# Performance work log

Hardware: AMD Instinct MI355X
Metric: run time of the kernel (lower is better)

Reference implementation:

```python
import jax, jax.numpy as jnp
import numpy as np

N = 8192
IN_FEATS = 512
OUT_FEATS = 64
NEG_SLOPE = 0.01  # torch nn.LeakyReLU default


def setup_inputs() -> dict:
    key = jax.random.key(0)
    k1, k2, k3, k4, k5, k6 = jax.random.split(key, 6)
    inputs = jax.random.normal(k1, (N, IN_FEATS), dtype=jnp.float32)
    adj_matrix = (jax.random.uniform(k2, (N, N)) < 0.01).astype(jnp.float32)
    eye_matrix = jnp.eye(N, dtype=jnp.float32)
    # nn.Linear params (torch default init: U(-1/sqrt(in), 1/sqrt(in)))
    bound = 1.0 / np.sqrt(IN_FEATS)
    W = jax.random.uniform(k3, (OUT_FEATS, IN_FEATS), minval=-bound, maxval=bound, dtype=jnp.float32)
    b = jax.random.uniform(k4, (OUT_FEATS,), minval=-bound, maxval=bound, dtype=jnp.float32)
    # a_1, a_2 init: torch.rand -> U(0,1)
    a1 = jax.random.uniform(k5, (1, OUT_FEATS), dtype=jnp.float32)
    a2 = jax.random.uniform(k6, (1, OUT_FEATS), dtype=jnp.float32)
    return {"inputs": inputs, "adj_matrix": adj_matrix, "eye_matrix": eye_matrix,
            "W": W, "b": b, "a1": a1, "a2": a2}


def reference(inputs, adj_matrix, eye_matrix, W, b, a1, a2):
    z = inputs @ W.T + b                              # (N, out_feats)
    zi = jnp.sum(a1 * z, axis=1, keepdims=True)       # (N, 1)
    zj = jnp.sum(a2 * z, axis=1, keepdims=True)       # (N, 1)
    attention_A = adj_matrix * zi                     # row-broadcast, (N, N)
    attention_B = adj_matrix * (eye_matrix * zj)      # (N, N)
    attn = jax.nn.leaky_relu(attention_A + attention_B, negative_slope=NEG_SLOPE)
    attn = jax.nn.softmax(attn, axis=1)               # (N, N)
    h = z - attn @ z                                  # (N, out_feats)
    return jax.nn.relu(h)
```

## Files before the change

kernel.cpp:

```cpp
#include <hip/hip_runtime.h>
#include <math.h>

#define N 8192
#define INF 512
#define OUTF 64
#define NEG_SLOPE 0.01f

typedef float f32x4 __attribute__((ext_vector_type(4)));

__global__ __launch_bounds__(256) void k1_linear(
    const float* __restrict__ inputs, const float* __restrict__ W,
    const float* __restrict__ b, const float* __restrict__ a1,
    const float* __restrict__ a2,
    float* __restrict__ z, float* __restrict__ zi, float* __restrict__ zj,
    float* __restrict__ ztot)
{
    const int tid = threadIdx.x;
    const int f   = tid & 63;
    const int w   = tid >> 6;
    const int row0 = blockIdx.x * 8;

    __shared__ float part[4][8][64];
    __shared__ float ztot_l[64];
    if (tid < 64) ztot_l[tid] = 0.0f;

    float acc[8];
    #pragma unroll
    for (int r = 0; r < 8; ++r) acc[r] = 0.0f;

    const f32x4* wrow = (const f32x4*)(W + (size_t)f * INF + w * 128);
    const f32x4* irow = (const f32x4*)(inputs + (size_t)row0 * INF + w * 128);

    #pragma unroll 4
    for (int k4 = 0; k4 < 32; ++k4) {
        const f32x4 wv = wrow[k4];
        #pragma unroll
        for (int r = 0; r < 8; ++r) {
            const f32x4 iv = irow[(size_t)r * (INF / 4) + k4];
            acc[r] += wv.x * iv.x + wv.y * iv.y + wv.z * iv.z + wv.w * iv.w;
        }
    }
    #pragma unroll
    for (int r = 0; r < 8; ++r) part[w][r][f] = acc[r];
    __syncthreads();

    const float bias = b[f];
    const float a1f = a1[f], a2f = a2[f];
    float colsum = 0.0f;

    #pragma unroll
    for (int p = 0; p < 2; ++p) {
        const int r = w + p * 4;
        const float zv = part[0][r][f] + part[1][r][f] + part[2][r][f] + part[3][r][f] + bias;
        z[(size_t)(row0 + r) * OUTF + f] = zv;
        colsum += zv;
        float s1 = a1f * zv;
        float s2 = a2f * zv;
        #pragma unroll
        for (int m = 32; m > 0; m >>= 1) {
            s1 += __shfl_xor(s1, m, 64);
            s2 += __shfl_xor(s2, m, 64);
        }
        if (f == 0) { zi[row0 + r] = s1; zj[row0 + r] = s2; }
    }

    atomicAdd(&ztot_l[f], colsum);
    __syncthreads();
    if (tid < 64) atomicAdd(&ztot[tid], ztot_l[tid]);
}

__global__ __launch_bounds__(256) void k2_attn(
    const float* __restrict__ adj, const float* __restrict__ eye,
    const float* __restrict__ z, const float* __restrict__ zi,
    const float* __restrict__ zj, const float* __restrict__ ztot,
    float* __restrict__ out)
{
    const int i   = blockIdx.x;
    const int tid = threadIdx.x;

    __shared__ int   nzlist[768];
    __shared__ int   nnz_sh;
    __shared__ float aii_sh;
    __shared__ float part[4][64];

    if (tid == 0) { nnz_sh = 0; aii_sh = 0.0f; }
    __syncthreads();

    const f32x4* arow = (const f32x4*)(adj + (size_t)i * N);
    #pragma unroll
    for (int it = 0; it < 8; ++it) {
        const int v4 = tid + 256 * it;
        const f32x4 a = __builtin_nontemporal_load(arow + v4);
        const int j0 = v4 * 4;
        if (a.x != 0.0f) { int p = atomicAdd(&nnz_sh, 1); nzlist[p] = j0;     if (j0     == i) aii_sh = a.x; }
        if (a.y != 0.0f) { int p = atomicAdd(&nnz_sh, 1); nzlist[p] = j0 + 1; if (j0 + 1 == i) aii_sh = a.y; }
        if (a.z != 0.0f) { int p = atomicAdd(&nnz_sh, 1); nzlist[p] = j0 + 2; if (j0 + 2 == i) aii_sh = a.z; }
        if (a.w != 0.0f) { int p = atomicAdd(&nnz_sh, 1); nzlist[p] = j0 + 3; if (j0 + 3 == i) aii_sh = a.w; }
    }
    __syncthreads();

    const int   nnz = nnz_sh;
    const float aii = aii_sh;
    const int g = tid >> 6;
    const int f = tid & 63;

    float acc = 0.0f;
    for (int p = g; p < nnz; p += 4) {
        acc += z[(size_t)nzlist[p] * OUTF + f];
    }
    part[g][f] = acc;
    __syncthreads();

    if (tid < 64) {
        const float rowsum = part[0][f] + part[1][f] + part[2][f] + part[3][f];
        const float zii = zi[i];
        const float zji = zj[i];
        const float e   = eye[(size_t)i * N + i];
        const int   d   = (aii != 0.0f) ? 1 : 0;
        const float c   = (float)(nnz - d);

        const float v  = (zii > 0.0f) ? zii : NEG_SLOPE * zii;
        const float dp = aii * zii + aii * e * zji;
        const float dv = (dp > 0.0f) ? dp : NEG_SLOPE * dp;

        const float expv = expf(v);
        const float expd = expf(dv);
        const float S = (float)(N - 1) - c + c * expv + expd;

        const float z_if = z[(size_t)i * OUTF + f];
        const float A = rowsum - aii * z_if;
        const float num = (expv - 1.0f) * A + (ztot[f] - z_if) + expd * z_if;
        const float h = z_if - num / S;
        out[(size_t)i * OUTF + f] = (h > 0.0f) ? h : 0.0f;
    }
}

extern "C" void kernel_launch(void* const* d_in, const int* in_sizes, int n_in,
                              void* d_out, int out_size, void* d_ws, size_t ws_size,
                              hipStream_t stream) {
    const float* inputs = (const float*)d_in[0];
    const float* adj    = (const float*)d_in[1];
    const float* eye    = (const float*)d_in[2];
    const float* W      = (const float*)d_in[3];
    const float* b      = (const float*)d_in[4];
    const float* a1     = (const float*)d_in[5];
    const float* a2     = (const float*)d_in[6];
    float* out = (float*)d_out;

    float* z    = (float*)d_ws;
    float* zi   = z + (size_t)N * OUTF;
    float* zj   = zi + N;
    float* ztot = zj + N;

    (void)hipMemsetAsync(ztot, 0, OUTF * sizeof(float), stream);
    k1_linear<<<N / 8, 256, 0, stream>>>(inputs, W, b, a1, a2, z, zi, zj, ztot);
    k2_attn<<<N, 256, 0, stream>>>(adj, eye, z, zi, zj, ztot, out);
}
```

Before: 551.6 us.

## Process one adjacency row per wavefront using ballot-based nonzero gathering

```diff
diff --git a/kernel.cpp b/kernel.cpp
--- a/kernel.cpp
+++ b/kernel.cpp
@@ -13,7 +13,7 @@
     const float* __restrict__ b, const float* __restrict__ a1,
     const float* __restrict__ a2,
     float* __restrict__ z, float* __restrict__ zi, float* __restrict__ zj,
-    float* __restrict__ ztot)
+    float* __restrict__ ztot8)
 {
     const int tid = threadIdx.x;
     const int f   = tid & 63;
@@ -66,73 +66,92 @@
 
     atomicAdd(&ztot_l[f], colsum);
     __syncthreads();
-    if (tid < 64) atomicAdd(&ztot[tid], ztot_l[tid]);
+    if (tid < 64) atomicAdd(&ztot8[((blockIdx.x & 7) << 6) + tid], ztot_l[tid]);
+}
+
+__device__ __forceinline__ void proc_comp(float val, int base4, int c,
+                                          int i, int lane,
+                                          const float* __restrict__ z,
+                                          float& acc, float& aii, int& cnt)
+{
+    unsigned long long m = __ballot(val != 0.0f);
+    while (m) {
+        const int s = __ffsll(m) - 1;
+        m &= m - 1;
+        const int j = ((base4 + s) << 2) + c;
+        if (j == i) {
+            aii = __shfl(val, s, 64);
+        } else {
+            acc += z[(size_t)j * OUTF + lane];
+            ++cnt;
+        }
+    }
 }
 
 __global__ __launch_bounds__(256) void k2_attn(
     const float* __restrict__ adj, const float* __restrict__ eye,
     const float* __restrict__ z, const float* __restrict__ zi,
-    const float* __restrict__ zj, const float* __restrict__ ztot,
+    const float* __restrict__ zj, const float* __restrict__ ztot8,
     float* __restrict__ out)
 {
-    const int i   = blockIdx.x;
-    const int tid = threadIdx.x;
-
-    __shared__ int   nzlist[768];
-    __shared__ int   nnz_sh;
-    __shared__ float aii_sh;
-    __shared__ float part[4][64];
-
-    if (tid == 0) { nnz_sh = 0; aii_sh = 0.0f; }
-    __syncthreads();
+    const int lane = threadIdx.x & 63;
+    const int i    = (blockIdx.x << 2) + (threadIdx.x >> 6);
 
     const f32x4* arow = (const f32x4*)(adj + (size_t)i * N);
-    #pragma unroll
-    for (int it = 0; it < 8; ++it) {
-        const int v4 = tid + 256 * it;
-        const f32x4 a = __builtin_nontemporal_load(arow + v4);
-        const int j0 = v4 * 4;
-        if (a.x != 0.0f) { int p = atomicAdd(&nnz_sh, 1); nzlist[p] = j0;     if (j0     == i) aii_sh = a.x; }
-        if (a.y != 0.0f) { int p = atomicAdd(&nnz_sh, 1); nzlist[p] = j0 + 1; if (j0 + 1 == i) aii_sh = a.y; }
-        if (a.z != 0.0f) { int p = atomicAdd(&nnz_sh, 1); nzlist[p] = j0 + 2; if (j0 + 2 == i) aii_sh = a.z; }
-        if (a.w != 0.0f) { int p = atomicAdd(&nnz_sh, 1); nzlist[p] = j0 + 3; if (j0 + 3 == i) aii_sh = a.w; }
-    }
-    __syncthreads();
-
-    const int   nnz = nnz_sh;
-    const float aii = aii_sh;
-    const int g = tid >> 6;
-    const int f = tid & 63;
 
     float acc = 0.0f;
-    for (int p = g; p < nnz; p += 4) {
-        acc += z[(size_t)nzlist[p] * OUTF + f];
+    float aii = 0.0f;
+    int   cnt = 0;
+
+    #pragma unroll 1
+    for (int it = 0; it < 2048; it += 256) {
+        const f32x4 a0 = __builtin_nontemporal_load(arow + it +   0 + lane);
+        const f32x4 a1v = __builtin_nontemporal_load(arow + it +  64 + lane);
+        const f32x4 a2v = __builtin_nontemporal_load(arow + it + 128 + lane);
+        const f32x4 a3v = __builtin_nontemporal_load(arow + it + 192 + lane);
+
+        proc_comp(a0.x,  it +   0, 0, i, lane, z, acc, aii, cnt);
+        proc_comp(a0.y,  it +   0, 1, i, lane, z, acc, aii, cnt);
+        proc_comp(a0.z,  it +   0, 2, i, lane, z, acc, aii, cnt);
+        proc_comp(a0.w,  it +   0, 3, i, lane, z, acc, aii, cnt);
+
+        proc_comp(a1v.x, it +  64, 0, i, lane, z, acc, aii, cnt);
+        proc_comp(a1v.y, it +  64, 1, i, lane, z, acc, aii, cnt);
+        proc_comp(a1v.z, it +  64, 2, i, lane, z, acc, aii, cnt);
+        proc_comp(a1v.w, it +  64, 3, i, lane, z, acc, aii, cnt);
+
+        proc_comp(a2v.x, it + 128, 0, i, lane, z, acc, aii, cnt);
+        proc_comp(a2v.y, it + 128, 1, i, lane, z, acc, aii, cnt);
+        proc_comp(a2v.z, it + 128, 2, i, lane, z, acc, aii, cnt);
+        proc_comp(a2v.w, it + 128, 3, i, lane, z, acc, aii, cnt);
+
+        proc_comp(a3v.x, it + 192, 0, i, lane, z, acc, aii, cnt);
+        proc_comp(a3v.y, it + 192, 1, i, lane, z, acc, aii, cnt);
+        proc_comp(a3v.z, it + 192, 2, i, lane, z, acc, aii, cnt);
+        proc_comp(a3v.w, it + 192, 3, i, lane, z, acc, aii, cnt);
     }
-    part[g][f] = acc;
-    __syncthreads();
 
-    if (tid < 64) {
-        const float rowsum = part[0][f] + part[1][f] + part[2][f] + part[3][f];
-        const float zii = zi[i];
-        const float zji = zj[i];
-        const float e   = eye[(size_t)i * N + i];
-        const int   d   = (aii != 0.0f) ? 1 : 0;
-        const float c   = (float)(nnz - d);
+    const float zii = zi[i];
+    const float zji = zj[i];
+    const float e   = eye[(size_t)i * N + i];
 
-        const float v  = (zii > 0.0f) ? zii : NEG_SLOPE * zii;
-        const float dp = aii * zii + aii * e * zji;
-        const float dv = (dp > 0.0f) ? dp : NEG_SLOPE * dp;
+    float ztf = 0.0f;
+    #pragma unroll
+    for (int s = 0; s < 8; ++s) ztf += ztot8[(s << 6) + lane];
 
-        const float expv = expf(v);
-        const float expd = expf(dv);
-        const float S = (float)(N - 1) - c + c * expv + expd;
+    const float cf = (float)cnt;
+    const float v  = (zii > 0.0f) ? zii : NEG_SLOPE * zii;
+    const float dp = aii * zii + aii * e * zji;
+    const float dv = (dp > 0.0f) ? dp : NEG_SLOPE * dp;
 
-        const float z_if = z[(size_t)i * OUTF + f];
-        const float A = rowsum - aii * z_if;
-        const float num = (expv - 1.0f) * A + (ztot[f] - z_if) + expd * z_if;
-        const float h = z_if - num / S;
-        out[(size_t)i * OUTF + f] = (h > 0.0f) ? h : 0.0f;
-    }
+    const float expv = expf(v);
+    const float expd = expf(dv);
+    const float S = (float)(N - 1) - cf + cf * expv + expd;
+
+    const float z_if = z[(size_t)i * OUTF + lane];
+    const float num = (expv - 1.0f) * acc + (ztf - z_if) + expd * z_if;
+    const float h = z_if - num / S;
+    out[(size_t)i * OUTF + lane] = (h > 0.0f) ? h : 0.0f;
 }
 
 extern "C" void kernel_launch(void* const* d_in, const int* in_sizes, int n_in,
@@ -147,12 +166,12 @@
     const float* a2     = (const float*)d_in[6];
     float* out = (float*)d_out;
 
-    float* z    = (float*)d_ws;
-    float* zi   = z + (size_t)N * OUTF;
-    float* zj   = zi + N;
-    float* ztot = zj + N;
+    float* z     = (float*)d_ws;
+    float* zi    = z + (size_t)N * OUTF;
+    float* zj    = zi + N;
+    float* ztot8 = zj + N;
 
-    (void)hipMemsetAsync(ztot, 0, OUTF * sizeof(float), stream);
-    k1_linear<<<N / 8, 256, 0, stream>>>(inputs, W, b, a1, a2, z, zi, zj, ztot);
-    k2_attn<<<N, 256, 0, stream>>>(adj, eye, z, zi, zj, ztot, out);
+    (void)hipMemsetAsync(ztot8, 0, 8 * OUTF * sizeof(float), stream);
+    k1_linear<<<N / 8, 256, 0, stream>>>(inputs, W, b, a1, a2, z, zi, zj, ztot8);
+    k2_attn<<<N / 4, 256, 0, stream>>>(adj, eye, z, zi, zj, ztot8, out);
 }
```

New measurement: 538.1 us. -2.4%, faster.
